# Kernel tuning notes

Hardware: AMD Instinct MI355X
Metric: run time of the kernel (lower is better)

## Reference

```python
import math
import jax, jax.numpy as jnp
import numpy as np

NUM_HEADS = 16
ROTARY_BASE = 10000.0
FMIN = -3.4028234663852886e+38  # torch uses -FLT_MAX as the blocked logit value


def setup_inputs() -> dict:
    key = jax.random.key(0)
    ks = jax.random.split(key, 4)
    B, S, D = 2, 2048, 2048
    x = jax.random.normal(ks[0], (B, S, D), dtype=jnp.float32)
    mask = jnp.ones((B, S), dtype=bool)
    # Linear params stored as [in, out] (transpose of torch's [out, in])
    w_in = jax.random.normal(ks[1], (D, 3 * D), dtype=jnp.float32) * 0.02
    b_in = jnp.zeros((3 * D,), dtype=jnp.float32)
    w_out = jax.random.normal(ks[2], (D, D), dtype=jnp.float32) * 0.02
    b_out = jnp.zeros((D,), dtype=jnp.float32)
    return {"x": x, "mask": mask, "w_in": w_in, "b_in": b_in,
            "w_out": w_out, "b_out": b_out}


def _rotate_half(t):
    # curated-transformers RotaryEmbeddings._rotate: [-x2, x1]
    h = t.shape[-1] // 2
    return jnp.concatenate([-t[..., h:], t[..., :h]], axis=-1)


def _rope_cos_sin(seq_len, width):
    # theta_i = base^(-2i/d); m_theta duplicated (rotate-half / NeoX layout)
    theta = ROTARY_BASE ** (-jnp.arange(0, width, 2, dtype=jnp.float32) / width)
    m_theta = jnp.arange(seq_len, dtype=jnp.float32)[:, None] * theta[None, :]
    m_theta = jnp.concatenate([m_theta, m_theta], axis=-1)  # [S, width]
    return jnp.cos(m_theta), jnp.sin(m_theta)


def reference(x, mask, w_in, b_in, w_out, b_out):
    B, S, D = x.shape
    H = NUM_HEADS
    Dh = D // H

    proj = x @ w_in + b_in                       # [B, S, 3D]
    q, k, v = jnp.split(proj, 3, axis=-1)
    split = lambda t: t.reshape(B, S, H, Dh).transpose(0, 2, 1, 3)  # [B,H,S,Dh]
    q, k, v = split(q), split(k), split(v)

    # rotary_fraction == 1.0 -> full-head rotary, default positions 0..S-1
    cos, sin = _rope_cos_sin(S, Dh)              # [S, Dh]
    cos = cos[None, None]
    sin = sin[None, None]
    q = cos * q + sin * _rotate_half(q)
    k = cos * k + sin * _rotate_half(k)

    scores = jnp.einsum('bhqd,bhkd->bhqk', q, k) / math.sqrt(Dh)
    # causal mask (use_causal_mask=True): strictly upper triangle blocked
    causal = jnp.triu(jnp.full((S, S), FMIN, dtype=scores.dtype), k=1)
    scores = scores + causal[None, None]
    # padding mask: (1 - mask) * -FLT_MAX, broadcast over heads and queries
    logit_mask = (1.0 - mask.astype(scores.dtype)) * FMIN
    scores = scores + logit_mask[:, None, None, :]

    attn_w = jax.nn.softmax(scores, axis=-1)
    attn = jnp.einsum('bhqk,bhkd->bhqd', attn_w, v)  # dropout_prob=0 (eval)
    attn = attn.transpose(0, 2, 1, 3).reshape(B, S, D)  # combine_heads
    return attn @ w_out + b_out
```

## Files before the change

kernel.cpp:

```cpp
#include <hip/hip_runtime.h>

typedef unsigned short ushort_t;
typedef unsigned int u32;
typedef short bf16x8 __attribute__((ext_vector_type(8)));
typedef float f32x4 __attribute__((ext_vector_type(4)));

__device__ __forceinline__ ushort_t f2bf(float f) {
  u32 u = __float_as_uint(f);
  u += 0x7FFFu + ((u >> 16) & 1u);
  return (ushort_t)(u >> 16);
}
__device__ __forceinline__ float bf2f(ushort_t h) {
  return __uint_as_float(((u32)h) << 16);
}

__device__ __forceinline__ void async_cp16(const void* g, void* l) {
  __builtin_amdgcn_global_load_lds(
      (const u32 __attribute__((address_space(1)))*)(unsigned long long)g,
      (u32 __attribute__((address_space(3)))*)(u32)(unsigned long long)l,
      16, 0, 0);
}

#define MFMA_BF16(a, b, c) __builtin_amdgcn_mfma_f32_16x16x32_bf16((a), (b), (c), 0, 0, 0)

#define KFENCE() __asm__ __volatile__("" ::: "memory")
#define KBAR()                    \
  do {                            \
    KFENCE();                     \
    __builtin_amdgcn_s_barrier(); \
    KFENCE();                     \
  } while (0)

__global__ void cvt_bf16_k(const float* __restrict__ in, ushort_t* __restrict__ out, int n4) {
  int i = blockIdx.x * blockDim.x + threadIdx.x;
  if (i >= n4) return;
  float4 v = ((const float4*)in)[i];
  unsigned long long p = (unsigned long long)f2bf(v.x)
                       | ((unsigned long long)f2bf(v.y) << 16)
                       | ((unsigned long long)f2bf(v.z) << 32)
                       | ((unsigned long long)f2bf(v.w) << 48);
  ((unsigned long long*)out)[i] = p;
}

__global__ void transpose_cvt_k(const float* __restrict__ in, ushort_t* __restrict__ out,
                                int R, int C) {
  __shared__ float t[32][33];
  int c0 = blockIdx.x * 32, r0 = blockIdx.y * 32;
  int tx = threadIdx.x, ty = threadIdx.y;
#pragma unroll
  for (int i = 0; i < 4; ++i)
    t[ty + i * 8][tx] = in[(size_t)(r0 + ty + i * 8) * C + c0 + tx];
  __syncthreads();
#pragma unroll
  for (int i = 0; i < 4; ++i)
    out[(size_t)(c0 + ty + i * 8) * R + r0 + tx] = f2bf(t[tx][ty + i * 8]);
}

__global__ void rope_swz_k(const ushort_t* __restrict__ q, const ushort_t* __restrict__ k,
                           ushort_t* __restrict__ qs, ushort_t* __restrict__ ks) {
  int row = blockIdx.x * 2 + (threadIdx.x >> 7);
  int d = threadIdx.x & 127;
  int s = row & 2047;
  int i = d & 63;
  float theta = __expf(-(float)i * 0.14391156831212876f);
  float mt = (float)s * theta;
  float sn, cs;
  sincosf(mt, &sn, &cs);
  size_t base = (size_t)row * 128;
  float qd = bf2f(q[base + d]), qp = bf2f(q[base + (d ^ 64)]);
  float kd = bf2f(k[base + d]), kp = bf2f(k[base + (d ^ 64)]);
  float rq = (d < 64) ? -qp : qp;
  float rk = (d < 64) ? -kp : kp;
  size_t bhb = (size_t)(row >> 11) * 262144;
  size_t qoff = bhb + (size_t)((s >> 5) * 4096 + ((d >> 5) * 2 + ((s >> 4) & 1)) * 512 +
                               (((d >> 3) & 3) * 16 + (s & 15)) * 8 + (d & 7));
  size_t koff = bhb + (size_t)((s >> 6) * 8192 + (d >> 5) * 2048 + ((s >> 4) & 3) * 512 +
                               ((d >> 3) & 3) * 128 + (s & 15) * 8 + (d & 7));
  const float scale2 = 0.08838834764831845f * 1.44269504088896340f;
  qs[qoff] = f2bf(scale2 * (cs * qd + sn * rq));
  ks[koff] = f2bf(cs * kd + sn * rk);
}

template <int MODE>
__global__ __launch_bounds__(256, 2) void gemm_bt_k(
    const ushort_t* __restrict__ A, const ushort_t* __restrict__ Bt,
    const float* __restrict__ bias, float* __restrict__ Cout,
    ushort_t* __restrict__ Qd, ushort_t* __restrict__ Kd, ushort_t* __restrict__ Vd,
    int M, int N, int K) {
  __shared__ ushort_t As[128 * 32];
  __shared__ ushort_t Bs[128 * 32];

  const int tid = threadIdx.x;
  const int w = tid >> 6, lane = tid & 63;
  const int quad = lane >> 4, l15 = lane & 15;
  const int m0 = blockIdx.y * 128, n0 = blockIdx.x * 128;
  const int wr = w >> 1, wc = w & 1;

  f32x4 acc[4][4] = {};

  for (int k0 = 0; k0 < K; k0 += 32) {
#pragma unroll
    for (int i = 0; i < 2; ++i) {
      int slot = (w * 2 + i) * 64 + lane;
      int row = slot >> 2, seg = slot & 3;
      async_cp16(A + (size_t)(m0 + row) * K + k0 + seg * 8, As + (size_t)(w * 2 + i) * 512);
      async_cp16(Bt + (size_t)(n0 + row) * K + k0 + seg * 8, Bs + (size_t)(w * 2 + i) * 512);
    }
    __syncthreads();

    bf16x8 a[4], b[4];
#pragma unroll
    for (int mt = 0; mt < 4; ++mt)
      a[mt] = *(const bf16x8*)(As + (wr * 64 + mt * 16 + l15) * 32 + quad * 8);
#pragma unroll
    for (int nt = 0; nt < 4; ++nt)
      b[nt] = *(const bf16x8*)(Bs + (wc * 64 + nt * 16 + l15) * 32 + quad * 8);
#pragma unroll
    for (int mt = 0; mt < 4; ++mt)
#pragma unroll
      for (int nt = 0; nt < 4; ++nt)
        acc[mt][nt] = MFMA_BF16(a[mt], b[nt], acc[mt][nt]);
    __syncthreads();
  }

  if (MODE == 0) {
#pragma unroll
    for (int mt = 0; mt < 4; ++mt)
#pragma unroll
      for (int nt = 0; nt < 4; ++nt) {
        int col = n0 + wc * 64 + nt * 16 + l15;
        float bv = bias[col];
#pragma unroll
        for (int r = 0; r < 4; ++r) {
          int row = m0 + wr * 64 + mt * 16 + quad * 4 + r;
          Cout[(size_t)row * N + col] = acc[mt][nt][r] + bv;
        }
      }
  } else {
#pragma unroll
    for (int mt = 0; mt < 4; ++mt)
#pragma unroll
      for (int nt = 0; nt < 4; ++nt) {
        int col = n0 + wc * 64 + nt * 16 + l15;
        int which = col >> 11;
        int rem = col & 2047;
        int h = rem >> 7, d = rem & 127;
        float bv = bias[col];
#pragma unroll
        for (int r = 0; r < 4; ++r) {
          int row = m0 + wr * 64 + mt * 16 + quad * 4 + r;
          int bb = row >> 11, s = row & 2047;
          size_t bhb = (size_t)(bb * 16 + h) * 262144;
          ushort_t val = f2bf(acc[mt][nt][r] + bv);
          if (which == 2) {
            size_t off = bhb + (size_t)((s >> 6) * 8192 + ((s >> 5) & 1) * 4096 +
                                        (d >> 4) * 512 + ((s >> 3) & 3) * 128 +
                                        (d & 15) * 8 + (s & 7));
            Vd[off] = val;
          } else {
            ushort_t* dst = (which == 0) ? Qd : Kd;
            dst[bhb + (size_t)s * 128 + d] = val;
          }
        }
      }
  }
}

__device__ __forceinline__ void stage_tile64(const ushort_t* gs, ushort_t* lbase,
                                             int w, int K, int k0) {
  ushort_t* l = lbase + w * 512;
#pragma unroll
  for (int c = 0; c < 4; ++c)
    async_cp16(gs + (size_t)(c * 64) * K + k0, l + c * 4096);
}

template <int MODE>
__global__ __launch_bounds__(512, 2) void gemm256_k(
    const ushort_t* __restrict__ A, const ushort_t* __restrict__ Bt,
    const float* __restrict__ bias, float* __restrict__ Cout,
    ushort_t* __restrict__ Qd, ushort_t* __restrict__ Kd, ushort_t* __restrict__ Vd,
    int M, int N, int K) {
  __shared__ ushort_t As[2][16384];
  __shared__ ushort_t Bs[2][16384];

  const int tid = threadIdx.x;
  const int w = tid >> 6, lane = tid & 63;
  const int quad = lane >> 4, l15 = lane & 15;
  const int wr = w >> 2, wc = w & 3;
  const int m0 = blockIdx.y * 256, n0 = blockIdx.x * 256;

  const int rr = (w << 3) + (lane >> 3);
  const int sw = ((lane & 7) ^ ((lane >> 3) & 7)) << 3;
  const ushort_t* Ags = A + (size_t)(m0 + rr) * K + sw;
  const ushort_t* Bgs = Bt + (size_t)(n0 + rr) * K + sw;

  f32x4 acc[8][4] = {};

  stage_tile64(Ags, As[0], w, K, 0);
  stage_tile64(Bgs, Bs[0], w, K, 0);
  stage_tile64(Ags, As[1], w, K, 64);
  stage_tile64(Bgs, Bs[1], w, K, 64);
  __asm__ __volatile__("s_waitcnt vmcnt(8)" ::: "memory");
  KBAR();

  const int NT = K >> 6;

  for (int t = 0; t < NT; ++t) {
    const ushort_t* Ab = As[t & 1];
    const ushort_t* Bb = Bs[t & 1];
    const bool pre = (t + 2) < NT;
    const int kpre = (t + 2) << 6;

    bf16x8 a[4][2], b0[2][2], b1[2][2];

#pragma unroll
    for (int q = 0; q < 4; ++q)
#pragma unroll
      for (int kk = 0; kk < 2; ++kk) {
        int row = wr * 128 + q * 16 + l15;
        int gr = ((kk << 2) | quad) ^ (l15 & 7);
        a[q][kk] = *(const bf16x8*)(Ab + row * 64 + gr * 8);
      }
#pragma unroll
    for (int n2 = 0; n2 < 2; ++n2)
#pragma unroll
      for (int kk = 0; kk < 2; ++kk) {
        int row = wc * 64 + n2 * 16 + l15;
        int gr = ((kk << 2) | quad) ^ (l15 & 7);
        b0[n2][kk] = *(const bf16x8*)(Bb + row * 64 + gr * 8);
      }
    KBAR();
    __builtin_amdgcn_s_setprio(1);
#pragma unroll
    for (int q = 0; q < 4; ++q)
#pragma unroll
      for (int n2 = 0; n2 < 2; ++n2)
#pragma unroll
        for (int kk = 0; kk < 2; ++kk)
          acc[q][n2] = MFMA_BF16(a[q][kk], b0[n2][kk], acc[q][n2]);
    __builtin_amdgcn_s_setprio(0);
    KBAR();

#pragma unroll
    for (int n2 = 0; n2 < 2; ++n2)
#pragma unroll
      for (int kk = 0; kk < 2; ++kk) {
        int row = wc * 64 + 32 + n2 * 16 + l15;
        int gr = ((kk << 2) | quad) ^ (l15 & 7);
        b1[n2][kk] = *(const bf16x8*)(Bb + row * 64 + gr * 8);
      }
    KBAR();
    __builtin_amdgcn_s_setprio(1);
#pragma unroll
    for (int q = 0; q < 4; ++q)
#pragma unroll
      for (int n2 = 0; n2 < 2; ++n2)
#pragma unroll
        for (int kk = 0; kk < 2; ++kk)
          acc[q][2 + n2] = MFMA_BF16(a[q][kk], b1[n2][kk], acc[q][2 + n2]);
    __builtin_amdgcn_s_setprio(0);
    KBAR();

#pragma unroll
    for (int q = 0; q < 4; ++q)
#pragma unroll
      for (int kk = 0; kk < 2; ++kk) {
        int row = wr * 128 + 64 + q * 16 + l15;
        int gr = ((kk << 2) | quad) ^ (l15 & 7);
        a[q][kk] = *(const bf16x8*)(Ab + row * 64 + gr * 8);
      }
    if (pre) stage_tile64(Bgs, Bs[t & 1], w, K, kpre);
    KBAR();
    __builtin_amdgcn_s_setprio(1);
#pragma unroll
    for (int q = 0; q < 4; ++q)
#pragma unroll
      for (int n2 = 0; n2 < 2; ++n2)
#pragma unroll
        for (int kk = 0; kk < 2; ++kk)
          acc[4 + q][n2] = MFMA_BF16(a[q][kk], b0[n2][kk], acc[4 + q][n2]);
    __builtin_amdgcn_s_setprio(0);
    KBAR();

    if (pre) stage_tile64(Ags, As[t & 1], w, K, kpre);
    KBAR();
    __builtin_amdgcn_s_setprio(1);
#pragma unroll
    for (int q = 0; q < 4; ++q)
#pragma unroll
      for (int n2 = 0; n2 < 2; ++n2)
#pragma unroll
        for (int kk = 0; kk < 2; ++kk)
          acc[4 + q][2 + n2] = MFMA_BF16(a[q][kk], b1[n2][kk], acc[4 + q][2 + n2]);
    __builtin_amdgcn_s_setprio(0);
    if (pre) {
      __asm__ __volatile__("s_waitcnt vmcnt(8)" ::: "memory");
    } else {
      __asm__ __volatile__("s_waitcnt vmcnt(0)" ::: "memory");
    }
    KBAR();
  }

  if (MODE == 0) {
#pragma unroll
    for (int mt = 0; mt < 8; ++mt)
#pragma unroll
      for (int nt = 0; nt < 4; ++nt) {
        int col = n0 + wc * 64 + nt * 16 + l15;
        float bv = bias[col];
#pragma unroll
        for (int r = 0; r < 4; ++r) {
          int row = m0 + wr * 128 + mt * 16 + quad * 4 + r;
          Cout[(size_t)row * N + col] = acc[mt][nt][r] + bv;
        }
      }
  } else {
#pragma unroll
    for (int mt = 0; mt < 8; ++mt)
#pragma unroll
      for (int nt = 0; nt < 4; ++nt) {
        int col = n0 + wc * 64 + nt * 16 + l15;
        int which = col >> 11;
        int rem = col & 2047;
        int h = rem >> 7, d = rem & 127;
        float bv = bias[col];
#pragma unroll
        for (int r = 0; r < 4; ++r) {
          int row = m0 + wr * 128 + mt * 16 + quad * 4 + r;
          int bb = row >> 11, s = row & 2047;
          size_t bhb = (size_t)(bb * 16 + h) * 262144;
          ushort_t val = f2bf(acc[mt][nt][r] + bv);
          if (which == 2) {
            size_t off = bhb + (size_t)((s >> 6) * 8192 + ((s >> 5) & 1) * 4096 +
                                        (d >> 4) * 512 + ((s >> 3) & 3) * 128 +
                                        (d & 15) * 8 + (s & 7));
            Vd[off] = val;
          } else {
            ushort_t* dst = (which == 0) ? Qd : Kd;
            dst[bhb + (size_t)s * 128 + d] = val;
          }
        }
      }
  }
}

__global__ __launch_bounds__(64, 3) void attn_flash_k(
    const ushort_t* __restrict__ Qs, const ushort_t* __restrict__ Ks,
    const ushort_t* __restrict__ Vs, ushort_t* __restrict__ Ob) {
  __shared__ ushort_t Pw[1024];

  const int lane = threadIdx.x & 63;
  const int quad = lane >> 4, l15 = lane & 15;
  const int n = blockIdx.x;
  const int bh = (n & 7) * 4 + ((n >> 3) & 3);
  const int sx = n >> 5;
  const int g = (sx & 1) ? (sx >> 1) : (127 - (sx >> 1));
  const int b = bh >> 4, h = bh & 15;
  const int q0 = g * 16;
  const int ktmax = g >> 2;
  const int G = g >> 1, mt = g & 1;
  const size_t bhb = (size_t)bh * 262144;

  bf16x8 qa[4];
#pragma unroll
  for (int kq = 0; kq < 4; ++kq)
    qa[kq] = *(const bf16x8*)(Qs + bhb + G * 4096 + (kq * 2 + mt) * 512 + lane * 8);

  f32x4 o[8] = {};
  float mi[4], li[4];
#pragma unroll
  for (int r = 0; r < 4; ++r) { mi[r] = -1e30f; li[r] = 0.f; }

  for (int kt = 0; kt <= ktmax; ++kt) {
    const int k0 = kt * 64;
    const ushort_t* kbase = Ks + bhb + (size_t)kt * 8192;
    const ushort_t* vbase = Vs + bhb + (size_t)kt * 8192;

    f32x4 sa[4] = {};
#pragma unroll
    for (int h2 = 0; h2 < 2; ++h2) {
      bf16x8 kb2[2][4];
#pragma unroll
      for (int kq = 0; kq < 2; ++kq)
#pragma unroll
        for (int nt = 0; nt < 4; ++nt)
          kb2[kq][nt] =
              *(const bf16x8*)(kbase + ((h2 * 2 + kq) * 4 + nt) * 512 + lane * 8);
#pragma unroll
      for (int kq = 0; kq < 2; ++kq)
#pragma unroll
        for (int nt = 0; nt < 4; ++nt)
          sa[nt] = MFMA_BF16(qa[h2 * 2 + kq], kb2[kq][nt], sa[nt]);
    }

    bf16x8 vb0[8];
#pragma unroll
    for (int nt = 0; nt < 8; ++nt)
      vb0[nt] = *(const bf16x8*)(vbase + nt * 512 + lane * 8);

    const bool diag = (kt == ktmax);
#pragma unroll
    for (int r = 0; r < 4; ++r) {
      int qg = q0 + quad * 4 + r;
      float sv[4];
      float rmax = -1e30f;
#pragma unroll
      for (int nt = 0; nt < 4; ++nt) {
        float vv = sa[nt][r];
        if (diag) { int kgc = k0 + nt * 16 + l15; if (kgc > qg) vv = -1e30f; }
        sv[nt] = vv;
        rmax = fmaxf(rmax, vv);
      }
      rmax = fmaxf(rmax, __shfl_xor(rmax, 1));
      rmax = fmaxf(rmax, __shfl_xor(rmax, 2));
      rmax = fmaxf(rmax, __shfl_xor(rmax, 4));
      rmax = fmaxf(rmax, __shfl_xor(rmax, 8));
      float mnew = fmaxf(mi[r], rmax);
      float alpha = exp2f(mi[r] - mnew);
      float psum = 0.f;
#pragma unroll
      for (int nt = 0; nt < 4; ++nt) {
        float p = exp2f(sv[nt] - mnew);
        psum += p;
        Pw[(nt >> 1) * 512 + (nt & 1) * 256 + (l15 >> 3) * 128 +
           quad * 32 + r * 8 + (l15 & 7)] = f2bf(p);
      }
      psum += __shfl_xor(psum, 1);
      psum += __shfl_xor(psum, 2);
      psum += __shfl_xor(psum, 4);
      psum += __shfl_xor(psum, 8);
      li[r] = li[r] * alpha + psum;
      mi[r] = mnew;
#pragma unroll
      for (int nt = 0; nt < 8; ++nt) o[nt][r] *= alpha;
    }

    __asm__ __volatile__("" ::: "memory");

    {
      bf16x8 pa = *(const bf16x8*)(Pw + lane * 8);
#pragma unroll
      for (int nt = 0; nt < 8; ++nt)
        o[nt] = MFMA_BF16(pa, vb0[nt], o[nt]);
    }
    {
      bf16x8 vb1[8];
#pragma unroll
      for (int nt = 0; nt < 8; ++nt)
        vb1[nt] = *(const bf16x8*)(vbase + (8 + nt) * 512 + lane * 8);
      bf16x8 pa = *(const bf16x8*)(Pw + 512 + lane * 8);
#pragma unroll
      for (int nt = 0; nt < 8; ++nt)
        o[nt] = MFMA_BF16(pa, vb1[nt], o[nt]);
    }
  }

#pragma unroll
  for (int r = 0; r < 4; ++r) {
    float inv = 1.f / li[r];
    int s = q0 + quad * 4 + r;
    size_t rowbase = ((size_t)b * 2048 + s) * 2048 + h * 128;
#pragma unroll
    for (int nt = 0; nt < 8; ++nt)
      Ob[rowbase + nt * 16 + l15] = f2bf(o[nt][r] * inv);
  }
}

extern "C" void kernel_launch(void* const* d_in, const int* in_sizes, int n_in,
                              void* d_out, int out_size, void* d_ws, size_t ws_size,
                              hipStream_t stream) {
  const float* x     = (const float*)d_in[0];
  const float* w_in  = (const float*)d_in[2];
  const float* b_in  = (const float*)d_in[3];
  const float* w_out = (const float*)d_in[4];
  const float* b_out = (const float*)d_in[5];
  float* out = (float*)d_out;

  ushort_t* x_bf    = (ushort_t*)d_ws;
  ushort_t* w_in_t  = x_bf + 8388608;
  ushort_t* w_out_t = w_in_t + 12582912;
  ushort_t* q       = w_out_t + 4194304;
  ushort_t* k       = q + 8388608;
  ushort_t* vswz    = k + 8388608;

  ushort_t* qswz = x_bf;
  ushort_t* kswz = w_in_t;
  ushort_t* attn = q;

  cvt_bf16_k<<<dim3(8192), dim3(256), 0, stream>>>(x, x_bf, 2097152);
  transpose_cvt_k<<<dim3(192, 64), dim3(32, 8), 0, stream>>>(w_in, w_in_t, 2048, 6144);
  transpose_cvt_k<<<dim3(64, 64), dim3(32, 8), 0, stream>>>(w_out, w_out_t, 2048, 2048);
  gemm256_k<1><<<dim3(24, 16), dim3(512), 0, stream>>>(
      x_bf, w_in_t, b_in, nullptr, q, k, vswz, 4096, 6144, 2048);
  rope_swz_k<<<dim3(32768), dim3(256), 0, stream>>>(q, k, qswz, kswz);
  attn_flash_k<<<dim3(4096), dim3(64), 0, stream>>>(qswz, kswz, vswz, attn);
  gemm_bt_k<0><<<dim3(16, 32), dim3(256), 0, stream>>>(
      attn, w_out_t, b_out, out, nullptr, nullptr, nullptr, 4096, 2048, 2048);
}
```

Baseline: 425.7 us.

## Unify GEMMs into triple-buffered 128x256 kernel with swizzled async staging

Replaces both the 256x256 QKV GEMM and the simple 128x128 output-projection GEMM with one 128x256-tile, 512-thread kernel. It uses a three-stage LDS ring with XOR-swizzled async global-to-LDS loads, and the prefetch for stage t+2 is issued early in iteration t. The QKV launch doubles its grid and the output projection moves from a single-buffered 32-wide K loop to the pipelined 64-wide path. This trades per-block reuse in the QKV GEMM for more blocks and a deeper prefetch, and it uses more LDS per block.

```diff
diff --git a/kernel.cpp b/kernel.cpp
--- a/kernel.cpp
+++ b/kernel.cpp
@@ -81,46 +81,118 @@
   ks[koff] = f2bf(cs * kd + sn * rk);
 }
 
+__device__ __forceinline__ void stage_chunks(const ushort_t* gs, ushort_t* lbase,
+                                             int w, int K, int k0, int nchunk) {
+  ushort_t* l = lbase + w * 512;
+  if (nchunk == 2) {
+#pragma unroll
+    for (int c = 0; c < 2; ++c)
+      async_cp16(gs + (size_t)(c * 64) * K + k0, l + c * 4096);
+  } else {
+#pragma unroll
+    for (int c = 0; c < 4; ++c)
+      async_cp16(gs + (size_t)(c * 64) * K + k0, l + c * 4096);
+  }
+}
+
 template <int MODE>
-__global__ __launch_bounds__(256, 2) void gemm_bt_k(
+__global__ __launch_bounds__(512) void gemm_dp_k(
     const ushort_t* __restrict__ A, const ushort_t* __restrict__ Bt,
     const float* __restrict__ bias, float* __restrict__ Cout,
     ushort_t* __restrict__ Qd, ushort_t* __restrict__ Kd, ushort_t* __restrict__ Vd,
     int M, int N, int K) {
-  __shared__ ushort_t As[128 * 32];
-  __shared__ ushort_t Bs[128 * 32];
+  __shared__ ushort_t As[3][8192];
+  __shared__ ushort_t Bs[3][16384];
 
   const int tid = threadIdx.x;
   const int w = tid >> 6, lane = tid & 63;
   const int quad = lane >> 4, l15 = lane & 15;
-  const int m0 = blockIdx.y * 128, n0 = blockIdx.x * 128;
-  const int wr = w >> 1, wc = w & 1;
+  const int wr = w >> 2, wc = w & 3;
+  const int m0 = blockIdx.y * 128, n0 = blockIdx.x * 256;
+
+  const int rr = (w << 3) + (lane >> 3);
+  const int sw = ((lane & 7) ^ ((lane >> 3) & 7)) << 3;
+  const ushort_t* Ags = A + (size_t)(m0 + rr) * K + sw;
+  const ushort_t* Bgs = Bt + (size_t)(n0 + rr) * K + sw;
 
   f32x4 acc[4][4] = {};
 
-  for (int k0 = 0; k0 < K; k0 += 32) {
-#pragma unroll
-    for (int i = 0; i < 2; ++i) {
-      int slot = (w * 2 + i) * 64 + lane;
-      int row = slot >> 2, seg = slot & 3;
-      async_cp16(A + (size_t)(m0 + row) * K + k0 + seg * 8, As + (size_t)(w * 2 + i) * 512);
-      async_cp16(Bt + (size_t)(n0 + row) * K + k0 + seg * 8, Bs + (size_t)(w * 2 + i) * 512);
-    }
-    __syncthreads();
-
-    bf16x8 a[4], b[4];
-#pragma unroll
-    for (int mt = 0; mt < 4; ++mt)
-      a[mt] = *(const bf16x8*)(As + (wr * 64 + mt * 16 + l15) * 32 + quad * 8);
-#pragma unroll
-    for (int nt = 0; nt < 4; ++nt)
-      b[nt] = *(const bf16x8*)(Bs + (wc * 64 + nt * 16 + l15) * 32 + quad * 8);
-#pragma unroll
-    for (int mt = 0; mt < 4; ++mt)
-#pragma unroll
-      for (int nt = 0; nt < 4; ++nt)
-        acc[mt][nt] = MFMA_BF16(a[mt], b[nt], acc[mt][nt]);
-    __syncthreads();
+  ushort_t *A0 = As[0], *A1 = As[1], *A2 = As[2];
+  ushort_t *B0 = Bs[0], *B1 = Bs[1], *B2 = Bs[2];
+
+  stage_chunks(Ags, A0, w, K, 0, 2);
+  stage_chunks(Bgs, B0, w, K, 0, 4);
+  stage_chunks(Ags, A1, w, K, 64, 2);
+  stage_chunks(Bgs, B1, w, K, 64, 4);
+  __asm__ __volatile__("s_waitcnt vmcnt(6)" ::: "memory");
+  KBAR();
+
+  const int NT = K >> 6;
+
+  for (int t = 0; t < NT; ++t) {
+    const bool pre = (t + 2) < NT;
+    const int kpre = (t + 2) << 6;
+
+    bf16x8 a[4][2], b0[2][2], b1[2][2];
+
+#pragma unroll
+    for (int mt = 0; mt < 4; ++mt)
+#pragma unroll
+      for (int kk = 0; kk < 2; ++kk) {
+        int row = wr * 64 + mt * 16 + l15;
+        int gr = ((kk << 2) | quad) ^ (l15 & 7);
+        a[mt][kk] = *(const bf16x8*)(A0 + row * 64 + gr * 8);
+      }
+#pragma unroll
+    for (int n2 = 0; n2 < 2; ++n2)
+#pragma unroll
+      for (int kk = 0; kk < 2; ++kk) {
+        int row = wc * 64 + n2 * 16 + l15;
+        int gr = ((kk << 2) | quad) ^ (l15 & 7);
+        b0[n2][kk] = *(const bf16x8*)(B0 + row * 64 + gr * 8);
+      }
+    if (pre) {
+      stage_chunks(Ags, A2, w, K, kpre, 2);
+      stage_chunks(Bgs, B2, w, K, kpre, 4);
+    }
+    KBAR();
+    __builtin_amdgcn_s_setprio(1);
+#pragma unroll
+    for (int mt = 0; mt < 4; ++mt)
+#pragma unroll
+      for (int n2 = 0; n2 < 2; ++n2)
+#pragma unroll
+        for (int kk = 0; kk < 2; ++kk)
+          acc[mt][n2] = MFMA_BF16(a[mt][kk], b0[n2][kk], acc[mt][n2]);
+    __builtin_amdgcn_s_setprio(0);
+    KBAR();
+
+#pragma unroll
+    for (int n2 = 0; n2 < 2; ++n2)
+#pragma unroll
+      for (int kk = 0; kk < 2; ++kk) {
+        int row = wc * 64 + 32 + n2 * 16 + l15;
+        int gr = ((kk << 2) | quad) ^ (l15 & 7);
+        b1[n2][kk] = *(const bf16x8*)(B0 + row * 64 + gr * 8);
+      }
+    KBAR();
+    __builtin_amdgcn_s_setprio(1);
+#pragma unroll
+    for (int mt = 0; mt < 4; ++mt)
+#pragma unroll
+      for (int n2 = 0; n2 < 2; ++n2)
+#pragma unroll
+        for (int kk = 0; kk < 2; ++kk)
+          acc[mt][2 + n2] = MFMA_BF16(a[mt][kk], b1[n2][kk], acc[mt][2 + n2]);
+    __builtin_amdgcn_s_setprio(0);
+    if (pre) {
+      __asm__ __volatile__("s_waitcnt vmcnt(6)" ::: "memory");
+    } else {
+      __asm__ __volatile__("s_waitcnt vmcnt(0)" ::: "memory");
+    }
+    KBAR();
+    ushort_t* tA = A0; A0 = A1; A1 = A2; A2 = tA;
+    ushort_t* tB = B0; B0 = B1; B1 = B2; B2 = tB;
   }
 
   if (MODE == 0) {
@@ -166,184 +238,6 @@
   }
 }
 
-__device__ __forceinline__ void stage_tile64(const ushort_t* gs, ushort_t* lbase,
-                                             int w, int K, int k0) {
-  ushort_t* l = lbase + w * 512;
-#pragma unroll
-  for (int c = 0; c < 4; ++c)
-    async_cp16(gs + (size_t)(c * 64) * K + k0, l + c * 4096);
-}
-
-template <int MODE>
-__global__ __launch_bounds__(512, 2) void gemm256_k(
-    const ushort_t* __restrict__ A, const ushort_t* __restrict__ Bt,
-    const float* __restrict__ bias, float* __restrict__ Cout,
-    ushort_t* __restrict__ Qd, ushort_t* __restrict__ Kd, ushort_t* __restrict__ Vd,
-    int M, int N, int K) {
-  __shared__ ushort_t As[2][16384];
-  __shared__ ushort_t Bs[2][16384];
-
-  const int tid = threadIdx.x;
-  const int w = tid >> 6, lane = tid & 63;
-  const int quad = lane >> 4, l15 = lane & 15;
-  const int wr = w >> 2, wc = w & 3;
-  const int m0 = blockIdx.y * 256, n0 = blockIdx.x * 256;
-
-  const int rr = (w << 3) + (lane >> 3);
-  const int sw = ((lane & 7) ^ ((lane >> 3) & 7)) << 3;
-  const ushort_t* Ags = A + (size_t)(m0 + rr) * K + sw;
-  const ushort_t* Bgs = Bt + (size_t)(n0 + rr) * K + sw;
-
-  f32x4 acc[8][4] = {};
-
-  stage_tile64(Ags, As[0], w, K, 0);
-  stage_tile64(Bgs, Bs[0], w, K, 0);
-  stage_tile64(Ags, As[1], w, K, 64);
-  stage_tile64(Bgs, Bs[1], w, K, 64);
-  __asm__ __volatile__("s_waitcnt vmcnt(8)" ::: "memory");
-  KBAR();
-
-  const int NT = K >> 6;
-
-  for (int t = 0; t < NT; ++t) {
-    const ushort_t* Ab = As[t & 1];
-    const ushort_t* Bb = Bs[t & 1];
-    const bool pre = (t + 2) < NT;
-    const int kpre = (t + 2) << 6;
-
-    bf16x8 a[4][2], b0[2][2], b1[2][2];
-
-#pragma unroll
-    for (int q = 0; q < 4; ++q)
-#pragma unroll
-      for (int kk = 0; kk < 2; ++kk) {
-        int row = wr * 128 + q * 16 + l15;
-        int gr = ((kk << 2) | quad) ^ (l15 & 7);
-        a[q][kk] = *(const bf16x8*)(Ab + row * 64 + gr * 8);
-      }
-#pragma unroll
-    for (int n2 = 0; n2 < 2; ++n2)
-#pragma unroll
-      for (int kk = 0; kk < 2; ++kk) {
-        int row = wc * 64 + n2 * 16 + l15;
-        int gr = ((kk << 2) | quad) ^ (l15 & 7);
-        b0[n2][kk] = *(const bf16x8*)(Bb + row * 64 + gr * 8);
-      }
-    KBAR();
-    __builtin_amdgcn_s_setprio(1);
-#pragma unroll
-    for (int q = 0; q < 4; ++q)
-#pragma unroll
-      for (int n2 = 0; n2 < 2; ++n2)
-#pragma unroll
-        for (int kk = 0; kk < 2; ++kk)
-          acc[q][n2] = MFMA_BF16(a[q][kk], b0[n2][kk], acc[q][n2]);
-    __builtin_amdgcn_s_setprio(0);
-    KBAR();
-
-#pragma unroll
-    for (int n2 = 0; n2 < 2; ++n2)
-#pragma unroll
-      for (int kk = 0; kk < 2; ++kk) {
-        int row = wc * 64 + 32 + n2 * 16 + l15;
-        int gr = ((kk << 2) | quad) ^ (l15 & 7);
-        b1[n2][kk] = *(const bf16x8*)(Bb + row * 64 + gr * 8);
-      }
-    KBAR();
-    __builtin_amdgcn_s_setprio(1);
-#pragma unroll
-    for (int q = 0; q < 4; ++q)
-#pragma unroll
-      for (int n2 = 0; n2 < 2; ++n2)
-#pragma unroll
-        for (int kk = 0; kk < 2; ++kk)
-          acc[q][2 + n2] = MFMA_BF16(a[q][kk], b1[n2][kk], acc[q][2 + n2]);
-    __builtin_amdgcn_s_setprio(0);
-    KBAR();
-
-#pragma unroll
-    for (int q = 0; q < 4; ++q)
-#pragma unroll
-      for (int kk = 0; kk < 2; ++kk) {
-        int row = wr * 128 + 64 + q * 16 + l15;
-        int gr = ((kk << 2) | quad) ^ (l15 & 7);
-        a[q][kk] = *(const bf16x8*)(Ab + row * 64 + gr * 8);
-      }
-    if (pre) stage_tile64(Bgs, Bs[t & 1], w, K, kpre);
-    KBAR();
-    __builtin_amdgcn_s_setprio(1);
-#pragma unroll
-    for (int q = 0; q < 4; ++q)
-#pragma unroll
-      for (int n2 = 0; n2 < 2; ++n2)
-#pragma unroll
-        for (int kk = 0; kk < 2; ++kk)
-          acc[4 + q][n2] = MFMA_BF16(a[q][kk], b0[n2][kk], acc[4 + q][n2]);
-    __builtin_amdgcn_s_setprio(0);
-    KBAR();
-
-    if (pre) stage_tile64(Ags, As[t & 1], w, K, kpre);
-    KBAR();
-    __builtin_amdgcn_s_setprio(1);
-#pragma unroll
-    for (int q = 0; q < 4; ++q)
-#pragma unroll
-      for (int n2 = 0; n2 < 2; ++n2)
-#pragma unroll
-        for (int kk = 0; kk < 2; ++kk)
-          acc[4 + q][2 + n2] = MFMA_BF16(a[q][kk], b1[n2][kk], acc[4 + q][2 + n2]);
-    __builtin_amdgcn_s_setprio(0);
-    if (pre) {
-      __asm__ __volatile__("s_waitcnt vmcnt(8)" ::: "memory");
-    } else {
-      __asm__ __volatile__("s_waitcnt vmcnt(0)" ::: "memory");
-    }
-    KBAR();
-  }
-
-  if (MODE == 0) {
-#pragma unroll
-    for (int mt = 0; mt < 8; ++mt)
-#pragma unroll
-      for (int nt = 0; nt < 4; ++nt) {
-        int col = n0 + wc * 64 + nt * 16 + l15;
-        float bv = bias[col];
-#pragma unroll
-        for (int r = 0; r < 4; ++r) {
-          int row = m0 + wr * 128 + mt * 16 + quad * 4 + r;
-          Cout[(size_t)row * N + col] = acc[mt][nt][r] + bv;
-        }
-      }
-  } else {
-#pragma unroll
-    for (int mt = 0; mt < 8; ++mt)
-#pragma unroll
-      for (int nt = 0; nt < 4; ++nt) {
-        int col = n0 + wc * 64 + nt * 16 + l15;
-        int which = col >> 11;
-        int rem = col & 2047;
-        int h = rem >> 7, d = rem & 127;
-        float bv = bias[col];
-#pragma unroll
-        for (int r = 0; r < 4; ++r) {
-          int row = m0 + wr * 128 + mt * 16 + quad * 4 + r;
-          int bb = row >> 11, s = row & 2047;
-          size_t bhb = (size_t)(bb * 16 + h) * 262144;
-          ushort_t val = f2bf(acc[mt][nt][r] + bv);
-          if (which == 2) {
-            size_t off = bhb + (size_t)((s >> 6) * 8192 + ((s >> 5) & 1) * 4096 +
-                                        (d >> 4) * 512 + ((s >> 3) & 3) * 128 +
-                                        (d & 15) * 8 + (s & 7));
-            Vd[off] = val;
-          } else {
-            ushort_t* dst = (which == 0) ? Qd : Kd;
-            dst[bhb + (size_t)s * 128 + d] = val;
-          }
-        }
-      }
-  }
-}
-
 __global__ __launch_bounds__(64, 3) void attn_flash_k(
     const ushort_t* __restrict__ Qs, const ushort_t* __restrict__ Ks,
     const ushort_t* __restrict__ Vs, ushort_t* __restrict__ Ob) {
@@ -490,10 +384,10 @@
   cvt_bf16_k<<<dim3(8192), dim3(256), 0, stream>>>(x, x_bf, 2097152);
   transpose_cvt_k<<<dim3(192, 64), dim3(32, 8), 0, stream>>>(w_in, w_in_t, 2048, 6144);
   transpose_cvt_k<<<dim3(64, 64), dim3(32, 8), 0, stream>>>(w_out, w_out_t, 2048, 2048);
-  gemm256_k<1><<<dim3(24, 16), dim3(512), 0, stream>>>(
+  gemm_dp_k<1><<<dim3(24, 32), dim3(512), 0, stream>>>(
       x_bf, w_in_t, b_in, nullptr, q, k, vswz, 4096, 6144, 2048);
   rope_swz_k<<<dim3(32768), dim3(256), 0, stream>>>(q, k, qswz, kswz);
   attn_flash_k<<<dim3(4096), dim3(64), 0, stream>>>(qswz, kswz, vswz, attn);
-  gemm_bt_k<0><<<dim3(16, 32), dim3(256), 0, stream>>>(
+  gemm_dp_k<0><<<dim3(8, 32), dim3(512), 0, stream>>>(
       attn, w_out_t, b_out, out, nullptr, nullptr, nullptr, 4096, 2048, 2048);
 }
```

After: 427.6 us. No clear change (+0.4%).
